# Performance work log

Hardware: AMD Instinct MI355X
Metric: run time of the kernel (lower is better)

Reference implementation:

```python
import jax, jax.numpy as jnp
import numpy as np

NUM_HEADS = 4
NUM_GROUPS = 8
EPS = 1e-5


def setup_inputs() -> dict:
    key = jax.random.key(0)
    ks = jax.random.split(key, 5)
    B, C, H, W = 16, 512, 32, 32
    s = 1.0 / np.sqrt(C)
    return {
        "x": jax.random.normal(ks[0], (B, C, H, W), dtype=jnp.float32),
        "norm_w": jnp.ones((C,), jnp.float32),
        "norm_b": jnp.zeros((C,), jnp.float32),
        "q_w": jax.random.normal(ks[1], (C, C), jnp.float32) * s,
        "q_b": jnp.zeros((C,), jnp.float32),
        "k_w": jax.random.normal(ks[2], (C, C), jnp.float32) * s,
        "k_b": jnp.zeros((C,), jnp.float32),
        "v_w": jax.random.normal(ks[3], (C, C), jnp.float32) * s,
        "v_b": jnp.zeros((C,), jnp.float32),
        "p_w": jax.random.normal(ks[4], (C, C), jnp.float32) * s,
        "p_b": jnp.zeros((C,), jnp.float32),
    }


def _group_norm(x, w, b):
    # x: (B, C, N) -> GroupNorm over (C//G, N) per group
    B, C, N = x.shape
    g = x.reshape(B, NUM_GROUPS, C // NUM_GROUPS, N)
    mean = g.mean(axis=(2, 3), keepdims=True)
    var = g.var(axis=(2, 3), keepdims=True)
    g = (g - mean) * jax.lax.rsqrt(var + EPS)
    x = g.reshape(B, C, N)
    return x * w[None, :, None] + b[None, :, None]


def reference(x, norm_w, norm_b, q_w, q_b, k_w, k_b, v_w, v_b, p_w, p_b):
    B, C, H, W = x.shape
    N = H * W
    Ch = C // NUM_HEADS  # channels per head
    h = _group_norm(x.reshape(B, C, N), norm_w, norm_b)
    # 1x1 Conv1d == channel matmul: (o c, b c n -> b o n)
    q = jnp.einsum('oc,bcn->bon', q_w, h) + q_b[None, :, None]
    k = jnp.einsum('oc,bcn->bon', k_w, h) + k_b[None, :, None]
    v = jnp.einsum('oc,bcn->bon', v_w, h) + v_b[None, :, None]
    q = q.reshape(B, NUM_HEADS, Ch, N)
    k = k.reshape(B, NUM_HEADS, Ch, N)
    v = v.reshape(B, NUM_HEADS, Ch, N)
    attn = jnp.einsum('bhcn,bhcm->bhnm', q, k) * (1.0 / np.sqrt(Ch))
    attn = jax.nn.softmax(attn, axis=-1)
    out = jnp.einsum('bhnm,bhcm->bhcn', attn, v).reshape(B, C, N)
    out = jnp.einsum('oc,bcn->bon', p_w, out) + p_b[None, :, None]
    return x + out.reshape(B, C, H, W)
```

## Files before the change

### kernel.cpp

```cpp
#include <hip/hip_runtime.h>
#include <hip/hip_bf16.h>
#include <math.h>

#define B_    16
#define C_    512
#define N_    1024
#define G_    8
#define HEADS 4
#define CH    128
#define EPS   1e-5f

typedef __attribute__((ext_vector_type(8))) short short8;
typedef __attribute__((ext_vector_type(4))) float f32x4;
typedef __attribute__((ext_vector_type(16))) float f32x16;
typedef __attribute__((ext_vector_type(4))) int i32x4;

__device__ __forceinline__ unsigned short f2bf(float f) {
  union { float f; unsigned int i; } x; x.f = f;
  unsigned int r = x.i + 0x7FFFu + ((x.i >> 16) & 1u);
  return (unsigned short)(r >> 16);
}

__global__ __launch_bounds__(256) void gn_stats(const float* __restrict__ x,
                                                float* __restrict__ stats) {
  int bg = blockIdx.x;
  const float4* p4 = (const float4*)(x + (size_t)bg * (C_ / G_) * N_);
  const int n4 = (C_ / G_) * N_ / 4;
  float s = 0.f, ss = 0.f;
  for (int i = threadIdx.x; i < n4; i += 256) {
    float4 v = p4[i];
    s  += v.x + v.y + v.z + v.w;
    ss += v.x * v.x + v.y * v.y + v.z * v.z + v.w * v.w;
  }
  for (int o = 32; o; o >>= 1) { s += __shfl_down(s, o); ss += __shfl_down(ss, o); }
  __shared__ float ls[4], lss[4];
  int wid = threadIdx.x >> 6, lane = threadIdx.x & 63;
  if (lane == 0) { ls[wid] = s; lss[wid] = ss; }
  __syncthreads();
  if (threadIdx.x == 0) {
    float S = ls[0] + ls[1] + ls[2] + ls[3];
    float SS = lss[0] + lss[1] + lss[2] + lss[3];
    const float inv = 1.f / ((C_ / G_) * N_);
    float mean = S * inv;
    float var = SS * inv - mean * mean;
    stats[bg * 2]     = mean;
    stats[bg * 2 + 1] = rsqrtf(var + EPS);
  }
}

__global__ __launch_bounds__(256) void conv_w(const float* __restrict__ q, const float* __restrict__ k,
                                              const float* __restrict__ v, const float* __restrict__ p,
                                              const float* __restrict__ qb, const float* __restrict__ kb,
                                              unsigned short* __restrict__ dst,
                                              float* __restrict__ qkb) {
  const int n = C_ * C_;
  int i = blockIdx.x * 256 + threadIdx.x;
  if (i < n) {
    dst[i]         = f2bf(q[i]);
    dst[n + i]     = f2bf(k[i]);
    dst[2 * n + i] = f2bf(v[i]);
    dst[3 * n + i] = f2bf(p[i]);
  }
  if (i < 1024) qkb[i] = (i < 512) ? qb[i] : kb[i - 512];
}

__global__ __launch_bounds__(256) void gn_apply(const float* __restrict__ x,
                                                const float* __restrict__ stats,
                                                const float* __restrict__ gw,
                                                const float* __restrict__ gb,
                                                unsigned short* __restrict__ hT) {
  __shared__ float T[64][65];
  int b = blockIdx.z, c0 = blockIdx.y * 64, n0 = blockIdx.x * 64;
  int g = c0 / (C_ / G_);
  float mean = stats[(b * G_ + g) * 2], rstd = stats[(b * G_ + g) * 2 + 1];
  int t = threadIdx.x;
  for (int it = 0; it < 4; it++) {
    int L = it * 256 + t;
    int cc = L >> 4, nf = L & 15;
    float4 v = *(const float4*)&x[((size_t)b * C_ + c0 + cc) * N_ + n0 + nf * 4];
    float sw = gw[c0 + cc] * rstd, sb = gb[c0 + cc] - mean * sw;
    T[cc][nf * 4 + 0] = v.x * sw + sb;
    T[cc][nf * 4 + 1] = v.y * sw + sb;
    T[cc][nf * 4 + 2] = v.z * sw + sb;
    T[cc][nf * 4 + 3] = v.w * sw + sb;
  }
  __syncthreads();
  for (int it = 0; it < 4; it++) {
    int L = it * 256 + t;
    int nn = L >> 4, cv = L & 15;
    ushort4 o;
    o.x = f2bf(T[cv * 4 + 0][nn]);
    o.y = f2bf(T[cv * 4 + 1][nn]);
    o.z = f2bf(T[cv * 4 + 2][nn]);
    o.w = f2bf(T[cv * 4 + 3][nn]);
    *(ushort4*)&hT[((size_t)b * N_ + n0 + nn) * C_ + c0 + cv * 4] = o;
  }
}

template <bool OUT_BF16, bool BIAS_I, bool RESID>
__global__ __launch_bounds__(256) void gemm_tn(const unsigned short* __restrict__ A,
                                               const unsigned short* __restrict__ Bt,
                                               const float* __restrict__ bias,
                                               const float* __restrict__ resid,
                                               void* __restrict__ out,
                                               int Ncols, int K,
                                               long aBS, long bBS, long oBS) {
  __shared__ __align__(16) unsigned short As[128 * 64];
  __shared__ __align__(16) unsigned short Bs[128 * 64];
  const int b = blockIdx.z;
  const int i0 = blockIdx.y * 128, j0 = blockIdx.x * 128;
  const unsigned short* Ab = A + (size_t)b * aBS + (size_t)i0 * K;
  const unsigned short* Bb = Bt + (size_t)b * bBS + (size_t)j0 * K;
  const int t = threadIdx.x, w = t >> 6, l = t & 63;
  const int wi = (w >> 1) * 64, wj = (w & 1) * 64;
  const int lr = l & 15, lk = (l >> 4) * 8;
  const int srow = l >> 3, scol = (l & 7) * 8;

  f32x4 acc[4][4];
  const f32x4 zf = {0.f, 0.f, 0.f, 0.f};
#pragma unroll
  for (int m = 0; m < 4; m++)
#pragma unroll
    for (int n = 0; n < 4; n++) acc[m][n] = zf;

  for (int kt = 0; kt < K; kt += 64) {
    __syncthreads();
#pragma unroll
    for (int i = 0; i < 4; i++) {
      int seg = w * 4 + i;
      int row = seg * 8 + srow;
      __builtin_amdgcn_global_load_lds(
          (const __attribute__((address_space(1))) void*)&Ab[(size_t)row * K + kt + scol],
          (__attribute__((address_space(3))) void*)&As[seg * 512], 16, 0, 0);
      __builtin_amdgcn_global_load_lds(
          (const __attribute__((address_space(1))) void*)&Bb[(size_t)row * K + kt + scol],
          (__attribute__((address_space(3))) void*)&Bs[seg * 512], 16, 0, 0);
    }
    __syncthreads();
#pragma unroll
    for (int ks = 0; ks < 64; ks += 32) {
      short8 af[4], bf[4];
#pragma unroll
      for (int m = 0; m < 4; m++) af[m] = *(const short8*)&As[(wi + m * 16 + lr) * 64 + ks + lk];
#pragma unroll
      for (int n = 0; n < 4; n++) bf[n] = *(const short8*)&Bs[(wj + n * 16 + lr) * 64 + ks + lk];
#pragma unroll
      for (int m = 0; m < 4; m++)
#pragma unroll
        for (int n = 0; n < 4; n++)
          acc[m][n] = __builtin_amdgcn_mfma_f32_16x16x32_bf16(af[m], bf[n], acc[m][n], 0, 0, 0);
    }
  }

  int rbase = (l >> 4) * 4;
#pragma unroll
  for (int m = 0; m < 4; m++) {
    int ig = i0 + wi + m * 16 + rbase;
#pragma unroll
    for (int n = 0; n < 4; n++) {
      int jg = j0 + wj + n * 16 + lr;
#pragma unroll
      for (int r = 0; r < 4; r++) {
        float vv = acc[m][n][r];
        vv += BIAS_I ? bias[ig + r] : bias[jg];
        size_t oidx = (size_t)b * oBS + (size_t)(ig + r) * Ncols + jg;
        if (RESID) vv += resid[oidx];
        if (OUT_BF16) ((unsigned short*)out)[oidx] = f2bf(vv);
        else ((float*)out)[oidx] = vv;
      }
    }
  }
}

__global__ __launch_bounds__(256, 2) void attn_kernel(const unsigned short* __restrict__ qkT,
                                                      const unsigned short* __restrict__ v,
                                                      unsigned short* __restrict__ aoT) {
  __shared__ __align__(16) unsigned short Ks[2][64 * 128];
  __shared__ __align__(16) unsigned short Vs[2][128 * 64];
  const int t = threadIdx.x, w = t >> 6, l = t & 63;
  const int h = l >> 5, l31 = l & 31, l7 = l & 7;
  const int bh = blockIdx.y, b = bh >> 2, hd = bh & 3, c0h = hd * CH;
  const int qg = blockIdx.x * 128 + w * 32 + l31;
  const float sc2 = 0.08838834764831845f * 1.4426950408889634f;
  const float THRRAW = 11.5f / sc2;

  short8 qf[8];
  const unsigned short* qrow = qkT + ((size_t)b * N_ + qg) * 1024 + c0h;
#pragma unroll
  for (int kc = 0; kc < 8; kc++)
    qf[kc] = *(const short8*)&qrow[kc * 16 + h * 8];

  f32x16 o[4];
#pragma unroll
  for (int ct = 0; ct < 4; ct++) o[ct] = (f32x16)(0.f);
  float m = -INFINITY, lsum = 0.f;

  auto stage = [&](int cur, int tt) {
    int mt = tt * 64;
#pragma unroll
    for (int i = 0; i < 4; i++) {
      int seg = w * 4 + i;
      {
        int row = seg * 4 + (l >> 4);
        int gc = (l & 15) ^ (row & 7);
        const unsigned short* src = qkT + ((size_t)b * N_ + mt + row) * 1024 + 512 + c0h + gc * 8;
        __builtin_amdgcn_global_load_lds((const __attribute__((address_space(1))) void*)src,
                                         (__attribute__((address_space(3))) void*)&Ks[cur][seg * 512],
                                         16, 0, 0);
      }
      {
        int row = seg * 8 + (l >> 3);
        int gc = (l & 7) ^ (row & 7);
        const unsigned short* src = v + ((size_t)b * C_ + c0h + row) * N_ + mt + gc * 8;
        __builtin_amdgcn_global_load_lds((const __attribute__((address_space(1))) void*)src,
                                         (__attribute__((address_space(3))) void*)&Vs[cur][seg * 512],
                                         16, 0, 0);
      }
    }
  };

  stage(0, 0);

  for (int tt = 0; tt < 16; tt++) {
    int cur = tt & 1;
    __syncthreads();
    if (tt < 15) stage(cur ^ 1, tt + 1);

    f32x16 st0 = (f32x16)(0.f), st1 = (f32x16)(0.f);
    const unsigned short* KsB = &Ks[cur][0];
    __builtin_amdgcn_s_setprio(1);
#pragma unroll
    for (int kc = 0; kc < 8; kc++) {
      short8 kf0 = *(const short8*)&KsB[l31 * 128 + (((2 * kc + h) ^ l7) * 8)];
      short8 kf1 = *(const short8*)&KsB[(32 + l31) * 128 + (((2 * kc + h) ^ l7) * 8)];
      st0 = __builtin_amdgcn_mfma_f32_32x32x16_bf16(kf0, qf[kc], st0, 0, 0, 0);
      st1 = __builtin_amdgcn_mfma_f32_32x32x16_bf16(kf1, qf[kc], st1, 0, 0, 0);
    }
    __builtin_amdgcn_s_setprio(0);

    float tr[16];
#pragma unroll
    for (int r = 0; r < 16; r++) tr[r] = fmaxf(st0[r], st1[r]);
#pragma unroll
    for (int s = 8; s >= 1; s >>= 1)
#pragma unroll
      for (int r = 0; r < s; r++) tr[r] = fmaxf(tr[r], tr[r + s]);
    float pmax = fmaxf(tr[0], __shfl_xor(tr[0], 32));

    bool defer = (pmax <= m + THRRAW);
    bool skip = __all(defer);
    float mnew = skip ? m : fmaxf(m, pmax);
    float alpha = skip ? 1.f : exp2f((m - mnew) * sc2);
    float mb = mnew * sc2;
    m = mnew;

    float psg[4];
    short8 pf[4];
#pragma unroll
    for (int g = 0; g < 4; g++) {
      const int e0 = (g & 1) * 8;
      float p0, p1, p2, p3, p4, p5, p6, p7;
      if (g < 2) {
        p0 = exp2f(fmaf(st0[e0 + 0], sc2, -mb)); p1 = exp2f(fmaf(st0[e0 + 1], sc2, -mb));
        p2 = exp2f(fmaf(st0[e0 + 2], sc2, -mb)); p3 = exp2f(fmaf(st0[e0 + 3], sc2, -mb));
        p4 = exp2f(fmaf(st0[e0 + 4], sc2, -mb)); p5 = exp2f(fmaf(st0[e0 + 5], sc2, -mb));
        p6 = exp2f(fmaf(st0[e0 + 6], sc2, -mb)); p7 = exp2f(fmaf(st0[e0 + 7], sc2, -mb));
      } else {
        p0 = exp2f(fmaf(st1[e0 + 0], sc2, -mb)); p1 = exp2f(fmaf(st1[e0 + 1], sc2, -mb));
        p2 = exp2f(fmaf(st1[e0 + 2], sc2, -mb)); p3 = exp2f(fmaf(st1[e0 + 3], sc2, -mb));
        p4 = exp2f(fmaf(st1[e0 + 4], sc2, -mb)); p5 = exp2f(fmaf(st1[e0 + 5], sc2, -mb));
        p6 = exp2f(fmaf(st1[e0 + 6], sc2, -mb)); p7 = exp2f(fmaf(st1[e0 + 7], sc2, -mb));
      }
      float s01 = p0 + p1, s23 = p2 + p3, s45 = p4 + p5, s67 = p6 + p7;
      psg[g] = (s01 + s23) + (s45 + s67);
      unsigned int x, x2, y, y2;
      asm("v_cvt_pk_bf16_f32 %0, %1, %2" : "=v"(x)  : "v"(p0), "v"(p1));
      asm("v_cvt_pk_bf16_f32 %0, %1, %2" : "=v"(x2) : "v"(p2), "v"(p3));
      asm("v_cvt_pk_bf16_f32 %0, %1, %2" : "=v"(y)  : "v"(p4), "v"(p5));
      asm("v_cvt_pk_bf16_f32 %0, %1, %2" : "=v"(y2) : "v"(p6), "v"(p7));
      asm("v_permlane32_swap_b32 %0, %1" : "+v"(x), "+v"(y));
      asm("v_permlane32_swap_b32 %0, %1" : "+v"(x2), "+v"(y2));
      i32x4 pwv = {(int)x, (int)x2, (int)y, (int)y2};
      pf[g] = __builtin_bit_cast(short8, pwv);
    }
    float ps = (psg[0] + psg[1]) + (psg[2] + psg[3]);
    ps += __shfl_xor(ps, 32);
    lsum = lsum * alpha + ps;

    if (!skip) {
#pragma unroll
      for (int ct = 0; ct < 4; ct++)
#pragma unroll
        for (int r = 0; r < 16; r++) o[ct][r] *= alpha;
    }

    const unsigned short* VsB = &Vs[cur][0];
    __builtin_amdgcn_s_setprio(1);
#pragma unroll
    for (int ct = 0; ct < 4; ct++) {
#pragma unroll
      for (int g = 0; g < 4; g++) {
        short8 vf = *(const short8*)&VsB[(ct * 32 + l31) * 64 + (((2 * g + h) ^ l7) * 8)];
        o[ct] = __builtin_amdgcn_mfma_f32_32x32x16_bf16(vf, pf[g], o[ct], 0, 0, 0);
      }
    }
    __builtin_amdgcn_s_setprio(0);
  }

  float rn = 1.f / lsum;
  unsigned short* orow = aoT + ((size_t)b * N_ + qg) * C_ + c0h;
#pragma unroll
  for (int ct = 0; ct < 4; ct++)
#pragma unroll
    for (int u = 0; u < 4; u++) {
      ushort4 ov;
      ov.x = f2bf(o[ct][u * 4 + 0] * rn);
      ov.y = f2bf(o[ct][u * 4 + 1] * rn);
      ov.z = f2bf(o[ct][u * 4 + 2] * rn);
      ov.w = f2bf(o[ct][u * 4 + 3] * rn);
      *(ushort4*)&orow[ct * 32 + u * 8 + h * 4] = ov;
    }
}

extern "C" void kernel_launch(void* const* d_in, const int* in_sizes, int n_in,
                              void* d_out, int out_size, void* d_ws, size_t ws_size,
                              hipStream_t stream) {
  const float* x  = (const float*)d_in[0];
  const float* nw = (const float*)d_in[1];
  const float* nb = (const float*)d_in[2];
  const float* qw = (const float*)d_in[3];
  const float* qb = (const float*)d_in[4];
  const float* kw = (const float*)d_in[5];
  const float* kb = (const float*)d_in[6];
  const float* vw = (const float*)d_in[7];
  const float* vb = (const float*)d_in[8];
  const float* pw = (const float*)d_in[9];
  const float* pb = (const float*)d_in[10];

  char* ws = (char*)d_ws;
  unsigned short* wbf  = (unsigned short*)ws;
  float*          stats = (float*)(ws + 0x200000);
  float*          qkb  = (float*)(ws + 0x200800);
  unsigned short* hT   = (unsigned short*)(ws + 0x201000);
  unsigned short* qkT  = (unsigned short*)(ws + 0x1201000);
  unsigned short* vv   = (unsigned short*)(ws + 0x3201000);
  unsigned short* aoT  = hT;

  const long NC = (long)N_ * C_;
  const int n_w = C_ * C_;

  gn_stats<<<B_ * G_, 256, 0, stream>>>(x, stats);
  conv_w<<<n_w / 256, 256, 0, stream>>>(qw, kw, vw, pw, qb, kb, wbf, qkb);
  gn_apply<<<dim3(N_ / 64, C_ / 64, B_), 256, 0, stream>>>(x, stats, nw, nb, hT);

  gemm_tn<true, false, false><<<dim3(1024 / 128, N_ / 128, B_), 256, 0, stream>>>(
      hT, wbf, qkb, nullptr, qkT, 1024, C_, NC, 0, (long)N_ * 1024);
  gemm_tn<true, true, false><<<dim3(N_ / 128, C_ / 128, B_), 256, 0, stream>>>(
      wbf + 2 * n_w, hT, vb, nullptr, vv, N_, C_, 0, NC, NC);

  attn_kernel<<<dim3(N_ / 128, B_ * HEADS), 256, 0, stream>>>(qkT, vv, aoT);

  gemm_tn<false, true, true><<<dim3(N_ / 128, C_ / 128, B_), 256, 0, stream>>>(
      wbf + 3 * n_w, aoT, pb, x, d_out, N_, C_, 0, NC, NC);
}
```

Measured before the change: 165.8 us.

## Pipeline attention QK with PV, remap grids for XCD locality, split GN stats

The attention kernel now computes the next tile's QK^T scores interleaved with the current tile's PV MFMAs. K is double-buffered, V triple-buffered, and one barrier is issued per iteration, so matrix work overlaps the softmax and loads. All GEMM and attention launches become 1D grids with a batch/head-major swizzle, apparently to keep a batch's tiles on the same XCD for L2 reuse. GroupNorm statistics are split into 512 partial-sum blocks instead of 128, and gn_apply finalises mean and rstd. The changes add LDS use (a third V buffer) and register pressure from holding next-tile scores, which may reduce occupancy.

```diff
diff --git a/kernel.cpp b/kernel.cpp
--- a/kernel.cpp
+++ b/kernel.cpp
@@ -21,13 +21,12 @@
   return (unsigned short)(r >> 16);
 }
 
-__global__ __launch_bounds__(256) void gn_stats(const float* __restrict__ x,
-                                                float* __restrict__ stats) {
-  int bg = blockIdx.x;
-  const float4* p4 = (const float4*)(x + (size_t)bg * (C_ / G_) * N_);
-  const int n4 = (C_ / G_) * N_ / 4;
+__global__ __launch_bounds__(256) void gn_part(const float* __restrict__ x,
+                                               float2* __restrict__ psum) {
+  int blk = blockIdx.x;
+  const float4* p4 = (const float4*)(x + (size_t)blk * 16384);
   float s = 0.f, ss = 0.f;
-  for (int i = threadIdx.x; i < n4; i += 256) {
+  for (int i = threadIdx.x; i < 4096; i += 256) {
     float4 v = p4[i];
     s  += v.x + v.y + v.z + v.w;
     ss += v.x * v.x + v.y * v.y + v.z * v.z + v.w * v.w;
@@ -38,13 +37,10 @@
   if (lane == 0) { ls[wid] = s; lss[wid] = ss; }
   __syncthreads();
   if (threadIdx.x == 0) {
-    float S = ls[0] + ls[1] + ls[2] + ls[3];
-    float SS = lss[0] + lss[1] + lss[2] + lss[3];
-    const float inv = 1.f / ((C_ / G_) * N_);
-    float mean = S * inv;
-    float var = SS * inv - mean * mean;
-    stats[bg * 2]     = mean;
-    stats[bg * 2 + 1] = rsqrtf(var + EPS);
+    float2 r;
+    r.x = (ls[0] + ls[1]) + (ls[2] + ls[3]);
+    r.y = (lss[0] + lss[1]) + (lss[2] + lss[3]);
+    psum[blk] = r;
   }
 }
 
@@ -65,14 +61,19 @@
 }
 
 __global__ __launch_bounds__(256) void gn_apply(const float* __restrict__ x,
-                                                const float* __restrict__ stats,
+                                                const float2* __restrict__ psum,
                                                 const float* __restrict__ gw,
                                                 const float* __restrict__ gb,
                                                 unsigned short* __restrict__ hT) {
   __shared__ float T[64][65];
   int b = blockIdx.z, c0 = blockIdx.y * 64, n0 = blockIdx.x * 64;
-  int g = c0 / (C_ / G_);
-  float mean = stats[(b * G_ + g) * 2], rstd = stats[(b * G_ + g) * 2 + 1];
+  int bg = b * G_ + (c0 >> 6);
+  float2 p0 = psum[bg * 4 + 0], p1 = psum[bg * 4 + 1];
+  float2 p2 = psum[bg * 4 + 2], p3 = psum[bg * 4 + 3];
+  const float inv = 1.f / ((C_ / G_) * N_);
+  float mean = ((p0.x + p1.x) + (p2.x + p3.x)) * inv;
+  float var  = ((p0.y + p1.y) + (p2.y + p3.y)) * inv - mean * mean;
+  float rstd = rsqrtf(var + EPS);
   int t = threadIdx.x;
   for (int it = 0; it < 4; it++) {
     int L = it * 256 + t;
@@ -107,8 +108,11 @@
                                                long aBS, long bBS, long oBS) {
   __shared__ __align__(16) unsigned short As[128 * 64];
   __shared__ __align__(16) unsigned short Bs[128 * 64];
-  const int b = blockIdx.z;
-  const int i0 = blockIdx.y * 128, j0 = blockIdx.x * 128;
+  const int lin = blockIdx.x;
+  const int b = (lin & 7) * 2 + ((lin >> 3) & 1);
+  const int rest = lin >> 4;
+  const int bx = rest & 7, by = rest >> 3;
+  const int i0 = by * 128, j0 = bx * 128;
   const unsigned short* Ab = A + (size_t)b * aBS + (size_t)i0 * K;
   const unsigned short* Bb = Bt + (size_t)b * bBS + (size_t)j0 * K;
   const int t = threadIdx.x, w = t >> 6, l = t & 63;
@@ -176,59 +180,61 @@
                                                       const unsigned short* __restrict__ v,
                                                       unsigned short* __restrict__ aoT) {
   __shared__ __align__(16) unsigned short Ks[2][64 * 128];
-  __shared__ __align__(16) unsigned short Vs[2][128 * 64];
+  __shared__ __align__(16) unsigned short Vs[3][128 * 64];
   const int t = threadIdx.x, w = t >> 6, l = t & 63;
   const int h = l >> 5, l31 = l & 31, l7 = l & 7;
-  const int bh = blockIdx.y, b = bh >> 2, hd = bh & 3, c0h = hd * CH;
-  const int qg = blockIdx.x * 128 + w * 32 + l31;
+  const int lin = blockIdx.x;
+  const int bh = (lin & 7) * 8 + ((lin >> 3) & 7);
+  const int qt = lin >> 6;
+  const int b = bh >> 2, hd = bh & 3, c0h = hd * CH;
+  const int qg = qt * 128 + w * 32 + l31;
   const float sc2 = 0.08838834764831845f * 1.4426950408889634f;
   const float THRRAW = 11.5f / sc2;
 
   short8 qf[8];
   const unsigned short* qrow = qkT + ((size_t)b * N_ + qg) * 1024 + c0h;
 #pragma unroll
-  for (int kc = 0; kc < 8; kc++)
-    qf[kc] = *(const short8*)&qrow[kc * 16 + h * 8];
+  for (int kc = 0; kc < 8; kc++) qf[kc] = *(const short8*)&qrow[kc * 16 + h * 8];
 
   f32x16 o[4];
 #pragma unroll
   for (int ct = 0; ct < 4; ct++) o[ct] = (f32x16)(0.f);
   float m = -INFINITY, lsum = 0.f;
 
-  auto stage = [&](int cur, int tt) {
+  auto stageK = [&](int buf, int tt) {
     int mt = tt * 64;
 #pragma unroll
     for (int i = 0; i < 4; i++) {
       int seg = w * 4 + i;
-      {
-        int row = seg * 4 + (l >> 4);
-        int gc = (l & 15) ^ (row & 7);
-        const unsigned short* src = qkT + ((size_t)b * N_ + mt + row) * 1024 + 512 + c0h + gc * 8;
-        __builtin_amdgcn_global_load_lds((const __attribute__((address_space(1))) void*)src,
-                                         (__attribute__((address_space(3))) void*)&Ks[cur][seg * 512],
-                                         16, 0, 0);
-      }
-      {
-        int row = seg * 8 + (l >> 3);
-        int gc = (l & 7) ^ (row & 7);
-        const unsigned short* src = v + ((size_t)b * C_ + c0h + row) * N_ + mt + gc * 8;
-        __builtin_amdgcn_global_load_lds((const __attribute__((address_space(1))) void*)src,
-                                         (__attribute__((address_space(3))) void*)&Vs[cur][seg * 512],
-                                         16, 0, 0);
-      }
+      int row = seg * 4 + (l >> 4);
+      int gc = (l & 15) ^ (row & 7);
+      const unsigned short* src = qkT + ((size_t)b * N_ + mt + row) * 1024 + 512 + c0h + gc * 8;
+      __builtin_amdgcn_global_load_lds((const __attribute__((address_space(1))) void*)src,
+                                       (__attribute__((address_space(3))) void*)&Ks[buf][seg * 512],
+                                       16, 0, 0);
     }
   };
-
-  stage(0, 0);
-
-  for (int tt = 0; tt < 16; tt++) {
-    int cur = tt & 1;
-    __syncthreads();
-    if (tt < 15) stage(cur ^ 1, tt + 1);
-
-    f32x16 st0 = (f32x16)(0.f), st1 = (f32x16)(0.f);
-    const unsigned short* KsB = &Ks[cur][0];
-    __builtin_amdgcn_s_setprio(1);
+  auto stageV = [&](int buf, int tt) {
+    int mt = tt * 64;
+#pragma unroll
+    for (int i = 0; i < 4; i++) {
+      int seg = w * 4 + i;
+      int row = seg * 8 + (l >> 3);
+      int gc = (l & 7) ^ (row & 7);
+      const unsigned short* src = v + ((size_t)b * C_ + c0h + row) * N_ + mt + gc * 8;
+      __builtin_amdgcn_global_load_lds((const __attribute__((address_space(1))) void*)src,
+                                       (__attribute__((address_space(3))) void*)&Vs[buf][seg * 512],
+                                       16, 0, 0);
+    }
+  };
+
+  stageK(0, 0); stageV(0, 0);
+  stageK(1, 1); stageV(1, 1);
+  __syncthreads();
+
+  f32x16 st0 = (f32x16)(0.f), st1 = (f32x16)(0.f);
+  {
+    const unsigned short* KsB = &Ks[0][0];
 #pragma unroll
     for (int kc = 0; kc < 8; kc++) {
       short8 kf0 = *(const short8*)&KsB[l31 * 128 + (((2 * kc + h) ^ l7) * 8)];
@@ -236,7 +242,11 @@
       st0 = __builtin_amdgcn_mfma_f32_32x32x16_bf16(kf0, qf[kc], st0, 0, 0, 0);
       st1 = __builtin_amdgcn_mfma_f32_32x32x16_bf16(kf1, qf[kc], st1, 0, 0, 0);
     }
-    __builtin_amdgcn_s_setprio(0);
+  }
+  __syncthreads();
+
+  for (int tt = 0; tt < 16; tt++) {
+    if (tt < 14) { stageK(tt & 1, tt + 2); stageV((tt + 2) % 3, tt + 2); }
 
     float tr[16];
 #pragma unroll
@@ -247,8 +257,7 @@
       for (int r = 0; r < s; r++) tr[r] = fmaxf(tr[r], tr[r + s]);
     float pmax = fmaxf(tr[0], __shfl_xor(tr[0], 32));
 
-    bool defer = (pmax <= m + THRRAW);
-    bool skip = __all(defer);
+    bool skip = __all(pmax <= m + THRRAW);
     float mnew = skip ? m : fmaxf(m, pmax);
     float alpha = skip ? 1.f : exp2f((m - mnew) * sc2);
     float mb = mnew * sc2;
@@ -271,8 +280,7 @@
         p4 = exp2f(fmaf(st1[e0 + 4], sc2, -mb)); p5 = exp2f(fmaf(st1[e0 + 5], sc2, -mb));
         p6 = exp2f(fmaf(st1[e0 + 6], sc2, -mb)); p7 = exp2f(fmaf(st1[e0 + 7], sc2, -mb));
       }
-      float s01 = p0 + p1, s23 = p2 + p3, s45 = p4 + p5, s67 = p6 + p7;
-      psg[g] = (s01 + s23) + (s45 + s67);
+      psg[g] = ((p0 + p1) + (p2 + p3)) + ((p4 + p5) + (p6 + p7));
       unsigned int x, x2, y, y2;
       asm("v_cvt_pk_bf16_f32 %0, %1, %2" : "=v"(x)  : "v"(p0), "v"(p1));
       asm("v_cvt_pk_bf16_f32 %0, %1, %2" : "=v"(x2) : "v"(p2), "v"(p3));
@@ -294,17 +302,40 @@
         for (int r = 0; r < 16; r++) o[ct][r] *= alpha;
     }
 
-    const unsigned short* VsB = &Vs[cur][0];
+    const unsigned short* VsB = &Vs[tt % 3][0];
     __builtin_amdgcn_s_setprio(1);
-#pragma unroll
-    for (int ct = 0; ct < 4; ct++) {
-#pragma unroll
-      for (int g = 0; g < 4; g++) {
+    if (tt < 15) {
+      const unsigned short* KsN = &Ks[(tt + 1) & 1][0];
+      f32x16 nst0 = (f32x16)(0.f), nst1 = (f32x16)(0.f);
+#pragma unroll
+      for (int kc = 0; kc < 8; kc++) {
+        short8 kf0 = *(const short8*)&KsN[l31 * 128 + (((2 * kc + h) ^ l7) * 8)];
+        short8 kf1 = *(const short8*)&KsN[(32 + l31) * 128 + (((2 * kc + h) ^ l7) * 8)];
+        nst0 = __builtin_amdgcn_mfma_f32_32x32x16_bf16(kf0, qf[kc], nst0, 0, 0, 0);
+        nst1 = __builtin_amdgcn_mfma_f32_32x32x16_bf16(kf1, qf[kc], nst1, 0, 0, 0);
+        {
+          int p = 2 * kc;
+          int ct = p & 3, g = p >> 2;
+          short8 vf = *(const short8*)&VsB[(ct * 32 + l31) * 64 + (((2 * g + h) ^ l7) * 8)];
+          o[ct] = __builtin_amdgcn_mfma_f32_32x32x16_bf16(vf, pf[g], o[ct], 0, 0, 0);
+          p = 2 * kc + 1;
+          ct = p & 3; g = p >> 2;
+          vf = *(const short8*)&VsB[(ct * 32 + l31) * 64 + (((2 * g + h) ^ l7) * 8)];
+          o[ct] = __builtin_amdgcn_mfma_f32_32x32x16_bf16(vf, pf[g], o[ct], 0, 0, 0);
+        }
+      }
+      __builtin_amdgcn_s_setprio(0);
+      __syncthreads();
+      st0 = nst0; st1 = nst1;
+    } else {
+#pragma unroll
+      for (int p = 0; p < 16; p++) {
+        int ct = p & 3, g = p >> 2;
         short8 vf = *(const short8*)&VsB[(ct * 32 + l31) * 64 + (((2 * g + h) ^ l7) * 8)];
         o[ct] = __builtin_amdgcn_mfma_f32_32x32x16_bf16(vf, pf[g], o[ct], 0, 0, 0);
       }
-    }
-    __builtin_amdgcn_s_setprio(0);
+      __builtin_amdgcn_s_setprio(0);
+    }
   }
 
   float rn = 1.f / lsum;
@@ -339,27 +370,27 @@
 
   char* ws = (char*)d_ws;
   unsigned short* wbf  = (unsigned short*)ws;
-  float*          stats = (float*)(ws + 0x200000);
-  float*          qkb  = (float*)(ws + 0x200800);
-  unsigned short* hT   = (unsigned short*)(ws + 0x201000);
-  unsigned short* qkT  = (unsigned short*)(ws + 0x1201000);
-  unsigned short* vv   = (unsigned short*)(ws + 0x3201000);
+  float2*         psum = (float2*)(ws + 0x200000);
+  float*          qkb  = (float*)(ws + 0x201000);
+  unsigned short* hT   = (unsigned short*)(ws + 0x202000);
+  unsigned short* qkT  = (unsigned short*)(ws + 0x1202000);
+  unsigned short* vv   = (unsigned short*)(ws + 0x3202000);
   unsigned short* aoT  = hT;
 
   const long NC = (long)N_ * C_;
   const int n_w = C_ * C_;
 
-  gn_stats<<<B_ * G_, 256, 0, stream>>>(x, stats);
+  gn_part<<<512, 256, 0, stream>>>(x, psum);
   conv_w<<<n_w / 256, 256, 0, stream>>>(qw, kw, vw, pw, qb, kb, wbf, qkb);
-  gn_apply<<<dim3(N_ / 64, C_ / 64, B_), 256, 0, stream>>>(x, stats, nw, nb, hT);
-
-  gemm_tn<true, false, false><<<dim3(1024 / 128, N_ / 128, B_), 256, 0, stream>>>(
+  gn_apply<<<dim3(N_ / 64, C_ / 64, B_), 256, 0, stream>>>(x, psum, nw, nb, hT);
+
+  gemm_tn<true, false, false><<<dim3(1024), 256, 0, stream>>>(
       hT, wbf, qkb, nullptr, qkT, 1024, C_, NC, 0, (long)N_ * 1024);
-  gemm_tn<true, true, false><<<dim3(N_ / 128, C_ / 128, B_), 256, 0, stream>>>(
+  gemm_tn<true, true, false><<<dim3(512), 256, 0, stream>>>(
       wbf + 2 * n_w, hT, vb, nullptr, vv, N_, C_, 0, NC, NC);
 
-  attn_kernel<<<dim3(N_ / 128, B_ * HEADS), 256, 0, stream>>>(qkT, vv, aoT);
-
-  gemm_tn<false, true, true><<<dim3(N_ / 128, C_ / 128, B_), 256, 0, stream>>>(
+  attn_kernel<<<dim3(512), 256, 0, stream>>>(qkT, vv, aoT);
+
+  gemm_tn<false, true, true><<<dim3(512), 256, 0, stream>>>(
       wbf + 3 * n_w, aoT, pb, x, d_out, N_, C_, 0, NC, NC);
 }
```

After: 144.1 us. 1.15x faster.
